# Kernel tuning notes

Hardware: AMD Instinct MI355X
Metric: run time of the kernel (lower is better)

The kernel has to match this reference:

```python
import jax, jax.numpy as jnp
import numpy as np

N_NODES = 50000
N_EDGES = 800000
IN_DIM = 128
OUT_DIM = 64
BN_EPS = 1e-5
LRELU_SLOPE = 0.01


def setup_inputs() -> dict:
    key = jax.random.key(0)
    ks = jax.random.split(key, 8)
    feature = jax.random.normal(ks[0], (N_NODES, IN_DIM), dtype=jnp.float32)
    src = jax.random.randint(ks[1], (N_EDGES,), 0, N_NODES)
    dst = jax.random.randint(ks[2], (N_EDGES,), 0, N_NODES)
    edge_weight = jax.random.uniform(ks[3], (N_EDGES,), dtype=jnp.float32)
    # learned params
    b1 = jnp.zeros((IN_DIM,), jnp.float32)                      # gcn1 bias (weight=False)
    gamma1 = jnp.ones((IN_DIM,), jnp.float32)
    beta1 = jnp.zeros((IN_DIM,), jnp.float32)
    W2 = jax.random.normal(ks[4], (IN_DIM, OUT_DIM), jnp.float32) * (2.0 / IN_DIM) ** 0.5  # kaiming-ish
    b2 = jnp.zeros((OUT_DIM,), jnp.float32)
    gamma2 = jnp.ones((OUT_DIM,), jnp.float32)
    beta2 = jnp.zeros((OUT_DIM,), jnp.float32)
    return dict(feature=feature, edge_weight=edge_weight, b1=b1, gamma1=gamma1,
                beta1=beta1, W2=W2, b2=b2, gamma2=gamma2, beta2=beta2,
                src=src, dst=dst)


def _degrees(src, dst, n):
    ones = jnp.ones(src.shape[0], jnp.float32)
    deg_out = jnp.clip(jax.ops.segment_sum(ones, src, num_segments=n), 1.0)
    deg_in = jnp.clip(jax.ops.segment_sum(ones, dst, num_segments=n), 1.0)
    return deg_out, deg_in


def _graph_conv(x, src, dst, edge_w, W, b, deg_out, deg_in):
    # DGL GraphConv, norm='both': D_in^{-1/2} * A(_w) * D_out^{-1/2} * x (@ W) + b
    h = x * jax.lax.rsqrt(deg_out)[:, None]
    if W is not None:
        h = h @ W  # [N, out]
    m = h[src]                                   # gather  [E, d]
    if edge_w is not None:
        m = m * edge_w[:, None]
    agg = jax.ops.segment_sum(m, dst, num_segments=x.shape[0])  # scatter-add [N, d]
    return agg * jax.lax.rsqrt(deg_in)[:, None] + b


def _batchnorm(x, gamma, beta):
    mean = jnp.mean(x, axis=0)
    var = jnp.var(x, axis=0)  # biased, as torch BN training-mode normalization
    return gamma * (x - mean) * jax.lax.rsqrt(var + BN_EPS) + beta


def reference(feature, edge_weight, b1, gamma1, beta1, W2, b2, gamma2, beta2, src, dst):
    deg_out, deg_in = _degrees(src, dst, feature.shape[0])
    h = _graph_conv(feature, src, dst, edge_weight, None, b1, deg_out, deg_in)
    h = _batchnorm(h, gamma1, beta1)              # dropout = identity (eval)
    h1 = jnp.where(h > 0, h, LRELU_SLOPE * h)     # LeakyReLU
    h2 = _graph_conv(h1, src, dst, None, W2, b2, deg_out, deg_in)
    h = _batchnorm(h2, gamma2, beta2)
    return jax.nn.softmax(h, axis=-1)
```

## Files before the change

### kernel.cpp

```cpp
#include <hip/hip_runtime.h>
#include <cstddef>

typedef unsigned int u32;

#define N_NODES 50000
#define N_EDGES 800000
#define D1 128
#define D2 64
#define BN_EPS 1e-5f
#define LRELU 0.01f
#define ELLW 64
#define C1B 4096
#define C2B 4096

__device__ __forceinline__ u32 f2bf(float x) {
    u32 u = __float_as_uint(x);
    return (u + 0x7fffu + ((u >> 16) & 1u)) >> 16;
}
__device__ __forceinline__ float bflo(u32 p) { return __uint_as_float(p << 16); }
__device__ __forceinline__ float bfhi(u32 p) { return __uint_as_float(p & 0xffff0000u); }

__global__ void k_build(const int* __restrict__ src, const int* __restrict__ dst,
                        const float* __restrict__ ew, const float* __restrict__ feature,
                        int* __restrict__ cnt_in, int* __restrict__ cnt_out,
                        u32* __restrict__ ell, u32* __restrict__ feat_bf) {
    const int e = blockIdx.x * 256 + threadIdx.x;
    if (e < N_EDGES) {
        int d = dst[e];
        int slot = atomicAdd(&cnt_in[d], 1);
        if (slot < ELLW)
            ell[(size_t)d * ELLW + slot] = ((u32)src[e] << 16) | f2bf(ew[e]);
        atomicAdd(&cnt_out[src[e]], 1);
    }
    const int TOTU = N_NODES * (D1 / 2);
    for (int i = e; i < TOTU; i += N_EDGES) {
        float2 v = *(const float2*)&feature[2 * (size_t)i];
        feat_bf[i] = f2bf(v.x) | (f2bf(v.y) << 16);
    }
}

__global__ __launch_bounds__(128) void k_conv1(const u32* __restrict__ feat_bf,
                                               const int* __restrict__ cnt_in,
                                               const int* __restrict__ cnt_out,
                                               const u32* __restrict__ ell,
                                               const float* __restrict__ b1,
                                               float* __restrict__ t1,
                                               float* __restrict__ part1) {
    const int w = threadIdx.x >> 6, lane = threadIdx.x & 63;
    __shared__ int   s_idx[2][ELLW];
    __shared__ float s_sc[2][ELLW];
    __shared__ float red[2][D1];
    const float bb0 = b1[2 * lane], bb1 = b1[2 * lane + 1];
    float s0 = 0.f, q0 = 0.f, s1 = 0.f, q1 = 0.f;
    int cnt = cnt_in[blockIdx.x * 2 + w];
    int deg = min(cnt, ELLW);
    int  pf_i = 0; float pf_c = 0.f;
    if (lane < deg) {
        u32 ent = ell[(size_t)(blockIdx.x * 2 + w) * ELLW + lane];
        pf_i = ent >> 16;
        pf_c = bflo(ent) * rsqrtf((float)max(cnt_out[ent >> 16], 1));
    }
    for (int base = blockIdx.x * 2; base < N_NODES; base += 2 * C1B) {
        const int node = base + w;
        const int cdeg = deg, ccnt = cnt;
        if (lane < cdeg) { s_idx[w][lane] = pf_i; s_sc[w][lane] = pf_c; }
        const int nbase = base + 2 * C1B;
        if (nbase < N_NODES) {
            const int nnode = nbase + w;
            cnt = cnt_in[nnode];
            deg = min(cnt, ELLW);
            if (lane < deg) {
                u32 ent = ell[(size_t)nnode * ELLW + lane];
                pf_i = ent >> 16;
                pf_c = bflo(ent) * rsqrtf((float)max(cnt_out[ent >> 16], 1));
            }
        }
        float a0 = 0.f, a1 = 0.f, a2 = 0.f, a3 = 0.f;
        float a4 = 0.f, a5 = 0.f, a6 = 0.f, a7 = 0.f;
        int j = 0;
        for (; j + 7 < cdeg; j += 8) {
            u32 p0 = feat_bf[(size_t)s_idx[w][j]     * (D1 / 2) + lane];
            u32 p1 = feat_bf[(size_t)s_idx[w][j + 1] * (D1 / 2) + lane];
            u32 p2 = feat_bf[(size_t)s_idx[w][j + 2] * (D1 / 2) + lane];
            u32 p3 = feat_bf[(size_t)s_idx[w][j + 3] * (D1 / 2) + lane];
            u32 p4 = feat_bf[(size_t)s_idx[w][j + 4] * (D1 / 2) + lane];
            u32 p5 = feat_bf[(size_t)s_idx[w][j + 5] * (D1 / 2) + lane];
            u32 p6 = feat_bf[(size_t)s_idx[w][j + 6] * (D1 / 2) + lane];
            u32 p7 = feat_bf[(size_t)s_idx[w][j + 7] * (D1 / 2) + lane];
            float c0 = s_sc[w][j],     c1 = s_sc[w][j + 1];
            float c2 = s_sc[w][j + 2], c3 = s_sc[w][j + 3];
            float c4 = s_sc[w][j + 4], c5 = s_sc[w][j + 5];
            float c6 = s_sc[w][j + 6], c7 = s_sc[w][j + 7];
            a0 = fmaf(bflo(p0), c0, a0); a1 = fmaf(bfhi(p0), c0, a1);
            a2 = fmaf(bflo(p1), c1, a2); a3 = fmaf(bfhi(p1), c1, a3);
            a4 = fmaf(bflo(p2), c2, a4); a5 = fmaf(bfhi(p2), c2, a5);
            a6 = fmaf(bflo(p3), c3, a6); a7 = fmaf(bfhi(p3), c3, a7);
            a0 = fmaf(bflo(p4), c4, a0); a1 = fmaf(bfhi(p4), c4, a1);
            a2 = fmaf(bflo(p5), c5, a2); a3 = fmaf(bfhi(p5), c5, a3);
            a4 = fmaf(bflo(p6), c6, a4); a5 = fmaf(bfhi(p6), c6, a5);
            a6 = fmaf(bflo(p7), c7, a6); a7 = fmaf(bfhi(p7), c7, a7);
        }
        for (; j + 3 < cdeg; j += 4) {
            u32 p0 = feat_bf[(size_t)s_idx[w][j]     * (D1 / 2) + lane];
            u32 p1 = feat_bf[(size_t)s_idx[w][j + 1] * (D1 / 2) + lane];
            u32 p2 = feat_bf[(size_t)s_idx[w][j + 2] * (D1 / 2) + lane];
            u32 p3 = feat_bf[(size_t)s_idx[w][j + 3] * (D1 / 2) + lane];
            float c0 = s_sc[w][j],     c1 = s_sc[w][j + 1];
            float c2 = s_sc[w][j + 2], c3 = s_sc[w][j + 3];
            a0 = fmaf(bflo(p0), c0, a0); a1 = fmaf(bfhi(p0), c0, a1);
            a2 = fmaf(bflo(p1), c1, a2); a3 = fmaf(bfhi(p1), c1, a3);
            a4 = fmaf(bflo(p2), c2, a4); a5 = fmaf(bfhi(p2), c2, a5);
            a6 = fmaf(bflo(p3), c3, a6); a7 = fmaf(bfhi(p3), c3, a7);
        }
        for (; j < cdeg; ++j) {
            u32 p = feat_bf[(size_t)s_idx[w][j] * (D1 / 2) + lane];
            float c = s_sc[w][j];
            a0 = fmaf(bflo(p), c, a0); a1 = fmaf(bfhi(p), c, a1);
        }
        a0 += a2 + a4 + a6;
        a1 += a3 + a5 + a7;
        float r = rsqrtf((float)max(ccnt, 1));
        float v0 = a0 * r + bb0, v1 = a1 * r + bb1;
        float2 v = {v0, v1};
        *(float2*)&t1[(size_t)node * D1 + 2 * lane] = v;
        s0 += v0; q0 += v0 * v0; s1 += v1; q1 += v1 * v1;
    }
    red[w][2 * lane] = s0; red[w][2 * lane + 1] = s1;
    __syncthreads();
    if (w == 0) {
        part1[(size_t)blockIdx.x * 2 * D1 + 2 * lane]     = red[0][2 * lane] + red[1][2 * lane];
        part1[(size_t)blockIdx.x * 2 * D1 + 2 * lane + 1] = red[0][2 * lane + 1] + red[1][2 * lane + 1];
    }
    __syncthreads();
    red[w][2 * lane] = q0; red[w][2 * lane + 1] = q1;
    __syncthreads();
    if (w == 0) {
        part1[(size_t)blockIdx.x * 2 * D1 + D1 + 2 * lane]     = red[0][2 * lane] + red[1][2 * lane];
        part1[(size_t)blockIdx.x * 2 * D1 + D1 + 2 * lane + 1] = red[0][2 * lane + 1] + red[1][2 * lane + 1];
    }
}

template <int D>
__global__ __launch_bounds__(128) void k_bn_final(const float* __restrict__ part, int nblk,
                                                  const float* __restrict__ gamma,
                                                  const float* __restrict__ beta,
                                                  float* __restrict__ coef) {
    const int c = blockIdx.x;
    const int t = threadIdx.x;
    __shared__ float sh[4];
    float s = 0.f, q = 0.f;
    for (int b = t; b < nblk; b += 128) {
        s += part[(size_t)b * 2 * D + c];
        q += part[(size_t)b * 2 * D + D + c];
    }
    for (int o = 32; o >= 1; o >>= 1) {
        s += __shfl_xor(s, o, 64);
        q += __shfl_xor(q, o, 64);
    }
    if ((t & 63) == 0) { sh[(t >> 6) * 2] = s; sh[(t >> 6) * 2 + 1] = q; }
    __syncthreads();
    if (t == 0) {
        s = sh[0] + sh[2];
        q = sh[1] + sh[3];
        const float inv_n = 1.f / (float)N_NODES;
        float mean = s * inv_n;
        float var  = q * inv_n - mean * mean;
        float rstd = rsqrtf(var + BN_EPS);
        float a = gamma[c] * rstd;
        coef[c]     = a;
        coef[D + c] = beta[c] - mean * a;
    }
}

__global__ __launch_bounds__(256) void k_mm(const float* __restrict__ t1,
                                            const float* __restrict__ coef1,
                                            const int* __restrict__ cnt_out,
                                            const float* __restrict__ W2,
                                            u32* __restrict__ g_bf) {
    __shared__ float sW[D1 * D2];
    __shared__ float sX[32][132];
    const int tid = threadIdx.x;
    const int r0 = blockIdx.x * 32;
    for (int i = tid; i < D1 * D2 / 4; i += 256)
        ((float4*)sW)[i] = ((const float4*)W2)[i];
    for (int i = tid; i < 32 * (D1 / 4); i += 256) {
        int r = i >> 5, k4 = i & 31;
        int row = r0 + r;
        float4 v = {0.f, 0.f, 0.f, 0.f};
        if (row < N_NODES) {
            v = *(const float4*)&t1[(size_t)row * D1 + 4 * k4];
            float ro = rsqrtf((float)max(cnt_out[row], 1));
            int k = 4 * k4;
            float x;
            x = coef1[k]     * v.x + coef1[D1 + k];     v.x = ((x > 0.f) ? x : LRELU * x) * ro;
            x = coef1[k + 1] * v.y + coef1[D1 + k + 1]; v.y = ((x > 0.f) ? x : LRELU * x) * ro;
            x = coef1[k + 2] * v.z + coef1[D1 + k + 2]; v.z = ((x > 0.f) ? x : LRELU * x) * ro;
            x = coef1[k + 3] * v.w + coef1[D1 + k + 3]; v.w = ((x > 0.f) ? x : LRELU * x) * ro;
        }
        *(float4*)&sX[r][4 * k4] = v;
    }
    __syncthreads();
    const int c  = tid & 63;
    const int rg = tid >> 6;
    float acc[8] = {0.f, 0.f, 0.f, 0.f, 0.f, 0.f, 0.f, 0.f};
    for (int k = 0; k < D1; k += 4) {
        float w0 = sW[k * D2 + c];
        float w1 = sW[(k + 1) * D2 + c];
        float w2 = sW[(k + 2) * D2 + c];
        float w3 = sW[(k + 3) * D2 + c];
#pragma unroll
        for (int j = 0; j < 8; ++j) {
            float4 x4 = *(const float4*)&sX[rg + 4 * j][k];
            acc[j] = fmaf(x4.x, w0, acc[j]);
            acc[j] = fmaf(x4.y, w1, acc[j]);
            acc[j] = fmaf(x4.z, w2, acc[j]);
            acc[j] = fmaf(x4.w, w3, acc[j]);
        }
    }
#pragma unroll
    for (int j = 0; j < 8; ++j) {
        int row = r0 + rg + 4 * j;
        float partner = __shfl_xor(acc[j], 1, 64);
        if (row < N_NODES && (c & 1) == 0)
            g_bf[(size_t)row * (D2 / 2) + (c >> 1)] = f2bf(acc[j]) | (f2bf(partner) << 16);
    }
}

__global__ __launch_bounds__(128) void k_conv2(const u32* __restrict__ g_bf,
                                               const int* __restrict__ cnt_in,
                                               const u32* __restrict__ ell,
                                               const float* __restrict__ b2,
                                               float* __restrict__ out,
                                               float* __restrict__ part2) {
    const int w = threadIdx.x >> 6, lane = threadIdx.x & 63;
    const int m = lane & 31, half = lane >> 5;
    __shared__ int   s_idx[2][ELLW];
    __shared__ float red[2][D2];
    const float bb0 = b2[2 * m], bb1 = b2[2 * m + 1];
    float s0 = 0.f, q0 = 0.f, s1 = 0.f, q1 = 0.f;
    int cnt = cnt_in[blockIdx.x * 2 + w];
    int deg = min(cnt, ELLW);
    int pf_i = 0;
    if (lane < deg) pf_i = ell[(size_t)(blockIdx.x * 2 + w) * ELLW + lane] >> 16;
    for (int base = blockIdx.x * 2; base < N_NODES; base += 2 * C2B) {
        const int node = base + w;
        const int cdeg = deg, ccnt = cnt;
        if (lane < cdeg) s_idx[w][lane] = pf_i;
        const int nbase = base + 2 * C2B;
        if (nbase < N_NODES) {
            const int nnode = nbase + w;
            cnt = cnt_in[nnode];
            deg = min(cnt, ELLW);
            if (lane < deg) pf_i = ell[(size_t)nnode * ELLW + lane] >> 16;
        }
        float a0 = 0.f, a1 = 0.f, a2 = 0.f, a3 = 0.f;
        float a4 = 0.f, a5 = 0.f, a6 = 0.f, a7 = 0.f;
        int j = half;
        for (; j + 14 < cdeg; j += 16) {
            u32 p0 = g_bf[(size_t)s_idx[w][j]      * (D2 / 2) + m];
            u32 p1 = g_bf[(size_t)s_idx[w][j + 2]  * (D2 / 2) + m];
            u32 p2 = g_bf[(size_t)s_idx[w][j + 4]  * (D2 / 2) + m];
            u32 p3 = g_bf[(size_t)s_idx[w][j + 6]  * (D2 / 2) + m];
            u32 p4 = g_bf[(size_t)s_idx[w][j + 8]  * (D2 / 2) + m];
            u32 p5 = g_bf[(size_t)s_idx[w][j + 10] * (D2 / 2) + m];
            u32 p6 = g_bf[(size_t)s_idx[w][j + 12] * (D2 / 2) + m];
            u32 p7 = g_bf[(size_t)s_idx[w][j + 14] * (D2 / 2) + m];
            a0 += bflo(p0); a1 += bfhi(p0);
            a2 += bflo(p1); a3 += bfhi(p1);
            a4 += bflo(p2); a5 += bfhi(p2);
            a6 += bflo(p3); a7 += bfhi(p3);
            a0 += bflo(p4); a1 += bfhi(p4);
            a2 += bflo(p5); a3 += bfhi(p5);
            a4 += bflo(p6); a5 += bfhi(p6);
            a6 += bflo(p7); a7 += bfhi(p7);
        }
        for (; j + 6 < cdeg; j += 8) {
            u32 p0 = g_bf[(size_t)s_idx[w][j]     * (D2 / 2) + m];
            u32 p1 = g_bf[(size_t)s_idx[w][j + 2] * (D2 / 2) + m];
            u32 p2 = g_bf[(size_t)s_idx[w][j + 4] * (D2 / 2) + m];
            u32 p3 = g_bf[(size_t)s_idx[w][j + 6] * (D2 / 2) + m];
            a0 += bflo(p0); a1 += bfhi(p0);
            a2 += bflo(p1); a3 += bfhi(p1);
            a4 += bflo(p2); a5 += bfhi(p2);
            a6 += bflo(p3); a7 += bfhi(p3);
        }
        for (; j < cdeg; j += 2) {
            u32 p = g_bf[(size_t)s_idx[w][j] * (D2 / 2) + m];
            a0 += bflo(p); a1 += bfhi(p);
        }
        a0 += a2 + a4 + a6;
        a1 += a3 + a5 + a7;
        a0 += __shfl_xor(a0, 32, 64);
        a1 += __shfl_xor(a1, 32, 64);
        float r = rsqrtf((float)max(ccnt, 1));
        float v0 = a0 * r + bb0, v1 = a1 * r + bb1;
        if (half == 0) {
            float2 v = {v0, v1};
            *(float2*)&out[(size_t)node * D2 + 2 * m] = v;
            s0 += v0; q0 += v0 * v0; s1 += v1; q1 += v1 * v1;
        }
    }
    if (half == 0) { red[w][2 * m] = s0; red[w][2 * m + 1] = s1; }
    __syncthreads();
    if (w == 0 && half == 0) {
        part2[(size_t)blockIdx.x * 2 * D2 + 2 * m]     = red[0][2 * m] + red[1][2 * m];
        part2[(size_t)blockIdx.x * 2 * D2 + 2 * m + 1] = red[0][2 * m + 1] + red[1][2 * m + 1];
    }
    __syncthreads();
    if (half == 0) { red[w][2 * m] = q0; red[w][2 * m + 1] = q1; }
    __syncthreads();
    if (w == 0 && half == 0) {
        part2[(size_t)blockIdx.x * 2 * D2 + D2 + 2 * m]     = red[0][2 * m] + red[1][2 * m];
        part2[(size_t)blockIdx.x * 2 * D2 + D2 + 2 * m + 1] = red[0][2 * m + 1] + red[1][2 * m + 1];
    }
}

__global__ __launch_bounds__(256) void k_softmax(float* __restrict__ out,
                                                 const float* __restrict__ coef2) {
    const int tid = threadIdx.x;
    const int lane = tid & 63;
    const int row = blockIdx.x * 4 + (tid >> 6);
    if (row >= N_NODES) return;
    float v = out[(size_t)row * D2 + lane] * coef2[lane] + coef2[D2 + lane];
    float m = v;
    for (int o = 32; o >= 1; o >>= 1) m = fmaxf(m, __shfl_xor(m, o, 64));
    float e = expf(v - m);
    float s = e;
    for (int o = 32; o >= 1; o >>= 1) s += __shfl_xor(s, o, 64);
    out[(size_t)row * D2 + lane] = e / s;
}

extern "C" void kernel_launch(void* const* d_in, const int* in_sizes, int n_in,
                              void* d_out, int out_size, void* d_ws, size_t ws_size,
                              hipStream_t stream) {
    const float* feature = (const float*)d_in[0];
    const float* edge_w  = (const float*)d_in[1];
    const float* b1      = (const float*)d_in[2];
    const float* gamma1  = (const float*)d_in[3];
    const float* beta1   = (const float*)d_in[4];
    const float* W2      = (const float*)d_in[5];
    const float* b2      = (const float*)d_in[6];
    const float* gamma2  = (const float*)d_in[7];
    const float* beta2   = (const float*)d_in[8];
    const int*   src     = (const int*)d_in[9];
    const int*   dst     = (const int*)d_in[10];

    float* out = (float*)d_out;

    int*   cnt_in  = (int*)d_ws;
    int*   cnt_out = cnt_in + 50000;
    float* coef1   = (float*)(cnt_out + 50000);
    float* coef2   = coef1 + 256;
    float* part1   = coef2 + 128;
    u32*   ell     = (u32*)(part1 + 1048576);
    float* t1      = (float*)(ell + (size_t)N_NODES * ELLW);
    u32*   feat_bf = (u32*)(t1 + (size_t)N_NODES * D1);
    u32*   g_bf    = feat_bf;
    float* part2   = part1;

    hipMemsetAsync(cnt_in, 0, 2 * 50000 * sizeof(int), stream);

    const int EB = (N_EDGES + 255) / 256;
    k_build<<<EB, 256, 0, stream>>>(src, dst, edge_w, feature,
                                    cnt_in, cnt_out, ell, feat_bf);

    k_conv1<<<C1B, 128, 0, stream>>>(feat_bf, cnt_in, cnt_out, ell, b1, t1, part1);
    k_bn_final<D1><<<D1, 128, 0, stream>>>(part1, C1B, gamma1, beta1, coef1);

    k_mm<<<(N_NODES + 31) / 32, 256, 0, stream>>>(t1, coef1, cnt_out, W2, g_bf);

    k_conv2<<<C2B, 128, 0, stream>>>(g_bf, cnt_in, ell, b2, out, part2);
    k_bn_final<D2><<<D2, 128, 0, stream>>>(part2, C2B, gamma2, beta2, coef2);

    k_softmax<<<(N_NODES + 3) / 4, 256, 0, stream>>>(out, coef2);
}
```

Baseline: 210.8 us.

## Fuse conv1, BN, matmul, conv2 and softmax into one cooperative kernel

Replaces six separate launches (conv1, two BN finalizers, matmul, conv2, softmax) with one persistent cooperative kernel of 1024 blocks that separates the phases with grid-wide syncs. The goal is to remove per-launch overhead and launch gaps, and to shrink the partial-sum buffers, since BN now reduces over 1024 blocks instead of 4096. In exchange the grid is smaller, so per-block occupancy and latency hiding are lower. Grid syncs also add their own cost, the matmul tile shrinks to 8 rows, and the large static LDS allocation may limit how many blocks fit per CU.

```diff
diff --git a/kernel.cpp b/kernel.cpp
--- a/kernel.cpp
+++ b/kernel.cpp
@@ -1,6 +1,8 @@
 #include <hip/hip_runtime.h>
+#include <hip/hip_cooperative_groups.h>
 #include <cstddef>
 
+namespace cg = cooperative_groups;
 typedef unsigned int u32;
 
 #define N_NODES 50000
@@ -10,8 +12,7 @@
 #define BN_EPS 1e-5f
 #define LRELU 0.01f
 #define ELLW 64
-#define C1B 4096
-#define C2B 4096
+#define GRID 1024
 
 __device__ __forceinline__ u32 f2bf(float x) {
     u32 u = __float_as_uint(x);
@@ -39,129 +40,20 @@
     }
 }
 
-__global__ __launch_bounds__(128) void k_conv1(const u32* __restrict__ feat_bf,
-                                               const int* __restrict__ cnt_in,
-                                               const int* __restrict__ cnt_out,
-                                               const u32* __restrict__ ell,
-                                               const float* __restrict__ b1,
-                                               float* __restrict__ t1,
-                                               float* __restrict__ part1) {
-    const int w = threadIdx.x >> 6, lane = threadIdx.x & 63;
-    __shared__ int   s_idx[2][ELLW];
-    __shared__ float s_sc[2][ELLW];
-    __shared__ float red[2][D1];
-    const float bb0 = b1[2 * lane], bb1 = b1[2 * lane + 1];
-    float s0 = 0.f, q0 = 0.f, s1 = 0.f, q1 = 0.f;
-    int cnt = cnt_in[blockIdx.x * 2 + w];
-    int deg = min(cnt, ELLW);
-    int  pf_i = 0; float pf_c = 0.f;
-    if (lane < deg) {
-        u32 ent = ell[(size_t)(blockIdx.x * 2 + w) * ELLW + lane];
-        pf_i = ent >> 16;
-        pf_c = bflo(ent) * rsqrtf((float)max(cnt_out[ent >> 16], 1));
-    }
-    for (int base = blockIdx.x * 2; base < N_NODES; base += 2 * C1B) {
-        const int node = base + w;
-        const int cdeg = deg, ccnt = cnt;
-        if (lane < cdeg) { s_idx[w][lane] = pf_i; s_sc[w][lane] = pf_c; }
-        const int nbase = base + 2 * C1B;
-        if (nbase < N_NODES) {
-            const int nnode = nbase + w;
-            cnt = cnt_in[nnode];
-            deg = min(cnt, ELLW);
-            if (lane < deg) {
-                u32 ent = ell[(size_t)nnode * ELLW + lane];
-                pf_i = ent >> 16;
-                pf_c = bflo(ent) * rsqrtf((float)max(cnt_out[ent >> 16], 1));
-            }
-        }
-        float a0 = 0.f, a1 = 0.f, a2 = 0.f, a3 = 0.f;
-        float a4 = 0.f, a5 = 0.f, a6 = 0.f, a7 = 0.f;
-        int j = 0;
-        for (; j + 7 < cdeg; j += 8) {
-            u32 p0 = feat_bf[(size_t)s_idx[w][j]     * (D1 / 2) + lane];
-            u32 p1 = feat_bf[(size_t)s_idx[w][j + 1] * (D1 / 2) + lane];
-            u32 p2 = feat_bf[(size_t)s_idx[w][j + 2] * (D1 / 2) + lane];
-            u32 p3 = feat_bf[(size_t)s_idx[w][j + 3] * (D1 / 2) + lane];
-            u32 p4 = feat_bf[(size_t)s_idx[w][j + 4] * (D1 / 2) + lane];
-            u32 p5 = feat_bf[(size_t)s_idx[w][j + 5] * (D1 / 2) + lane];
-            u32 p6 = feat_bf[(size_t)s_idx[w][j + 6] * (D1 / 2) + lane];
-            u32 p7 = feat_bf[(size_t)s_idx[w][j + 7] * (D1 / 2) + lane];
-            float c0 = s_sc[w][j],     c1 = s_sc[w][j + 1];
-            float c2 = s_sc[w][j + 2], c3 = s_sc[w][j + 3];
-            float c4 = s_sc[w][j + 4], c5 = s_sc[w][j + 5];
-            float c6 = s_sc[w][j + 6], c7 = s_sc[w][j + 7];
-            a0 = fmaf(bflo(p0), c0, a0); a1 = fmaf(bfhi(p0), c0, a1);
-            a2 = fmaf(bflo(p1), c1, a2); a3 = fmaf(bfhi(p1), c1, a3);
-            a4 = fmaf(bflo(p2), c2, a4); a5 = fmaf(bfhi(p2), c2, a5);
-            a6 = fmaf(bflo(p3), c3, a6); a7 = fmaf(bfhi(p3), c3, a7);
-            a0 = fmaf(bflo(p4), c4, a0); a1 = fmaf(bfhi(p4), c4, a1);
-            a2 = fmaf(bflo(p5), c5, a2); a3 = fmaf(bfhi(p5), c5, a3);
-            a4 = fmaf(bflo(p6), c6, a4); a5 = fmaf(bfhi(p6), c6, a5);
-            a6 = fmaf(bflo(p7), c7, a6); a7 = fmaf(bfhi(p7), c7, a7);
-        }
-        for (; j + 3 < cdeg; j += 4) {
-            u32 p0 = feat_bf[(size_t)s_idx[w][j]     * (D1 / 2) + lane];
-            u32 p1 = feat_bf[(size_t)s_idx[w][j + 1] * (D1 / 2) + lane];
-            u32 p2 = feat_bf[(size_t)s_idx[w][j + 2] * (D1 / 2) + lane];
-            u32 p3 = feat_bf[(size_t)s_idx[w][j + 3] * (D1 / 2) + lane];
-            float c0 = s_sc[w][j],     c1 = s_sc[w][j + 1];
-            float c2 = s_sc[w][j + 2], c3 = s_sc[w][j + 3];
-            a0 = fmaf(bflo(p0), c0, a0); a1 = fmaf(bfhi(p0), c0, a1);
-            a2 = fmaf(bflo(p1), c1, a2); a3 = fmaf(bfhi(p1), c1, a3);
-            a4 = fmaf(bflo(p2), c2, a4); a5 = fmaf(bfhi(p2), c2, a5);
-            a6 = fmaf(bflo(p3), c3, a6); a7 = fmaf(bfhi(p3), c3, a7);
-        }
-        for (; j < cdeg; ++j) {
-            u32 p = feat_bf[(size_t)s_idx[w][j] * (D1 / 2) + lane];
-            float c = s_sc[w][j];
-            a0 = fmaf(bflo(p), c, a0); a1 = fmaf(bfhi(p), c, a1);
-        }
-        a0 += a2 + a4 + a6;
-        a1 += a3 + a5 + a7;
-        float r = rsqrtf((float)max(ccnt, 1));
-        float v0 = a0 * r + bb0, v1 = a1 * r + bb1;
-        float2 v = {v0, v1};
-        *(float2*)&t1[(size_t)node * D1 + 2 * lane] = v;
-        s0 += v0; q0 += v0 * v0; s1 += v1; q1 += v1 * v1;
-    }
-    red[w][2 * lane] = s0; red[w][2 * lane + 1] = s1;
-    __syncthreads();
-    if (w == 0) {
-        part1[(size_t)blockIdx.x * 2 * D1 + 2 * lane]     = red[0][2 * lane] + red[1][2 * lane];
-        part1[(size_t)blockIdx.x * 2 * D1 + 2 * lane + 1] = red[0][2 * lane + 1] + red[1][2 * lane + 1];
-    }
-    __syncthreads();
-    red[w][2 * lane] = q0; red[w][2 * lane + 1] = q1;
-    __syncthreads();
-    if (w == 0) {
-        part1[(size_t)blockIdx.x * 2 * D1 + D1 + 2 * lane]     = red[0][2 * lane] + red[1][2 * lane];
-        part1[(size_t)blockIdx.x * 2 * D1 + D1 + 2 * lane + 1] = red[0][2 * lane + 1] + red[1][2 * lane + 1];
-    }
-}
-
-template <int D>
-__global__ __launch_bounds__(128) void k_bn_final(const float* __restrict__ part, int nblk,
-                                                  const float* __restrict__ gamma,
-                                                  const float* __restrict__ beta,
-                                                  float* __restrict__ coef) {
-    const int c = blockIdx.x;
-    const int t = threadIdx.x;
-    __shared__ float sh[4];
+__device__ __forceinline__ void bnf_dev(const float* part, int nblk,
+                                        const float* gamma, const float* beta,
+                                        float* coef, int D, float* sh) {
+    const int c = blockIdx.x, t = threadIdx.x;
     float s = 0.f, q = 0.f;
     for (int b = t; b < nblk; b += 128) {
         s += part[(size_t)b * 2 * D + c];
         q += part[(size_t)b * 2 * D + D + c];
     }
-    for (int o = 32; o >= 1; o >>= 1) {
-        s += __shfl_xor(s, o, 64);
-        q += __shfl_xor(q, o, 64);
-    }
+    for (int o = 32; o >= 1; o >>= 1) { s += __shfl_xor(s, o, 64); q += __shfl_xor(q, o, 64); }
     if ((t & 63) == 0) { sh[(t >> 6) * 2] = s; sh[(t >> 6) * 2 + 1] = q; }
     __syncthreads();
     if (t == 0) {
-        s = sh[0] + sh[2];
-        q = sh[1] + sh[3];
+        s = sh[0] + sh[2]; q = sh[1] + sh[3];
         const float inv_n = 1.f / (float)N_NODES;
         float mean = s * inv_n;
         float var  = q * inv_n - mean * mean;
@@ -172,162 +64,287 @@
     }
 }
 
-__global__ __launch_bounds__(256) void k_mm(const float* __restrict__ t1,
-                                            const float* __restrict__ coef1,
-                                            const int* __restrict__ cnt_out,
-                                            const float* __restrict__ W2,
-                                            u32* __restrict__ g_bf) {
-    __shared__ float sW[D1 * D2];
-    __shared__ float sX[32][132];
+#define LDSB (32768 + 8 * 132 * 4)
+
+__global__ __launch_bounds__(128) void k_mega(const u32* __restrict__ feat_bf,
+                                              const int* __restrict__ cnt_in,
+                                              const int* __restrict__ cnt_out,
+                                              const u32* __restrict__ ell,
+                                              const float* __restrict__ b1,
+                                              float* __restrict__ t1,
+                                              float* __restrict__ part1,
+                                              const float* __restrict__ gamma1,
+                                              const float* __restrict__ beta1,
+                                              float* __restrict__ coef1,
+                                              const float* __restrict__ W2,
+                                              u32* __restrict__ g_bf,
+                                              const float* __restrict__ b2,
+                                              float* __restrict__ out,
+                                              float* __restrict__ part2,
+                                              const float* __restrict__ gamma2,
+                                              const float* __restrict__ beta2,
+                                              float* __restrict__ coef2) {
+    cg::grid_group grid = cg::this_grid();
+    __shared__ __align__(16) char lds[LDSB];
     const int tid = threadIdx.x;
-    const int r0 = blockIdx.x * 32;
-    for (int i = tid; i < D1 * D2 / 4; i += 256)
-        ((float4*)sW)[i] = ((const float4*)W2)[i];
-    for (int i = tid; i < 32 * (D1 / 4); i += 256) {
-        int r = i >> 5, k4 = i & 31;
-        int row = r0 + r;
-        float4 v = {0.f, 0.f, 0.f, 0.f};
-        if (row < N_NODES) {
-            v = *(const float4*)&t1[(size_t)row * D1 + 4 * k4];
-            float ro = rsqrtf((float)max(cnt_out[row], 1));
-            int k = 4 * k4;
-            float x;
-            x = coef1[k]     * v.x + coef1[D1 + k];     v.x = ((x > 0.f) ? x : LRELU * x) * ro;
-            x = coef1[k + 1] * v.y + coef1[D1 + k + 1]; v.y = ((x > 0.f) ? x : LRELU * x) * ro;
-            x = coef1[k + 2] * v.z + coef1[D1 + k + 2]; v.z = ((x > 0.f) ? x : LRELU * x) * ro;
-            x = coef1[k + 3] * v.w + coef1[D1 + k + 3]; v.w = ((x > 0.f) ? x : LRELU * x) * ro;
-        }
-        *(float4*)&sX[r][4 * k4] = v;
-    }
-    __syncthreads();
-    const int c  = tid & 63;
-    const int rg = tid >> 6;
-    float acc[8] = {0.f, 0.f, 0.f, 0.f, 0.f, 0.f, 0.f, 0.f};
-    for (int k = 0; k < D1; k += 4) {
-        float w0 = sW[k * D2 + c];
-        float w1 = sW[(k + 1) * D2 + c];
-        float w2 = sW[(k + 2) * D2 + c];
-        float w3 = sW[(k + 3) * D2 + c];
-#pragma unroll
-        for (int j = 0; j < 8; ++j) {
-            float4 x4 = *(const float4*)&sX[rg + 4 * j][k];
-            acc[j] = fmaf(x4.x, w0, acc[j]);
-            acc[j] = fmaf(x4.y, w1, acc[j]);
-            acc[j] = fmaf(x4.z, w2, acc[j]);
-            acc[j] = fmaf(x4.w, w3, acc[j]);
-        }
-    }
-#pragma unroll
-    for (int j = 0; j < 8; ++j) {
-        int row = r0 + rg + 4 * j;
-        float partner = __shfl_xor(acc[j], 1, 64);
-        if (row < N_NODES && (c & 1) == 0)
-            g_bf[(size_t)row * (D2 / 2) + (c >> 1)] = f2bf(acc[j]) | (f2bf(partner) << 16);
-    }
-}
-
-__global__ __launch_bounds__(128) void k_conv2(const u32* __restrict__ g_bf,
-                                               const int* __restrict__ cnt_in,
-                                               const u32* __restrict__ ell,
-                                               const float* __restrict__ b2,
-                                               float* __restrict__ out,
-                                               float* __restrict__ part2) {
-    const int w = threadIdx.x >> 6, lane = threadIdx.x & 63;
-    const int m = lane & 31, half = lane >> 5;
-    __shared__ int   s_idx[2][ELLW];
-    __shared__ float red[2][D2];
-    const float bb0 = b2[2 * m], bb1 = b2[2 * m + 1];
-    float s0 = 0.f, q0 = 0.f, s1 = 0.f, q1 = 0.f;
-    int cnt = cnt_in[blockIdx.x * 2 + w];
-    int deg = min(cnt, ELLW);
-    int pf_i = 0;
-    if (lane < deg) pf_i = ell[(size_t)(blockIdx.x * 2 + w) * ELLW + lane] >> 16;
-    for (int base = blockIdx.x * 2; base < N_NODES; base += 2 * C2B) {
-        const int node = base + w;
-        const int cdeg = deg, ccnt = cnt;
-        if (lane < cdeg) s_idx[w][lane] = pf_i;
-        const int nbase = base + 2 * C2B;
-        if (nbase < N_NODES) {
-            const int nnode = nbase + w;
-            cnt = cnt_in[nnode];
-            deg = min(cnt, ELLW);
-            if (lane < deg) pf_i = ell[(size_t)nnode * ELLW + lane] >> 16;
-        }
-        float a0 = 0.f, a1 = 0.f, a2 = 0.f, a3 = 0.f;
-        float a4 = 0.f, a5 = 0.f, a6 = 0.f, a7 = 0.f;
-        int j = half;
-        for (; j + 14 < cdeg; j += 16) {
-            u32 p0 = g_bf[(size_t)s_idx[w][j]      * (D2 / 2) + m];
-            u32 p1 = g_bf[(size_t)s_idx[w][j + 2]  * (D2 / 2) + m];
-            u32 p2 = g_bf[(size_t)s_idx[w][j + 4]  * (D2 / 2) + m];
-            u32 p3 = g_bf[(size_t)s_idx[w][j + 6]  * (D2 / 2) + m];
-            u32 p4 = g_bf[(size_t)s_idx[w][j + 8]  * (D2 / 2) + m];
-            u32 p5 = g_bf[(size_t)s_idx[w][j + 10] * (D2 / 2) + m];
-            u32 p6 = g_bf[(size_t)s_idx[w][j + 12] * (D2 / 2) + m];
-            u32 p7 = g_bf[(size_t)s_idx[w][j + 14] * (D2 / 2) + m];
-            a0 += bflo(p0); a1 += bfhi(p0);
-            a2 += bflo(p1); a3 += bfhi(p1);
-            a4 += bflo(p2); a5 += bfhi(p2);
-            a6 += bflo(p3); a7 += bfhi(p3);
-            a0 += bflo(p4); a1 += bfhi(p4);
-            a2 += bflo(p5); a3 += bfhi(p5);
-            a4 += bflo(p6); a5 += bfhi(p6);
-            a6 += bflo(p7); a7 += bfhi(p7);
-        }
-        for (; j + 6 < cdeg; j += 8) {
-            u32 p0 = g_bf[(size_t)s_idx[w][j]     * (D2 / 2) + m];
-            u32 p1 = g_bf[(size_t)s_idx[w][j + 2] * (D2 / 2) + m];
-            u32 p2 = g_bf[(size_t)s_idx[w][j + 4] * (D2 / 2) + m];
-            u32 p3 = g_bf[(size_t)s_idx[w][j + 6] * (D2 / 2) + m];
-            a0 += bflo(p0); a1 += bfhi(p0);
-            a2 += bflo(p1); a3 += bfhi(p1);
-            a4 += bflo(p2); a5 += bfhi(p2);
-            a6 += bflo(p3); a7 += bfhi(p3);
-        }
-        for (; j < cdeg; j += 2) {
-            u32 p = g_bf[(size_t)s_idx[w][j] * (D2 / 2) + m];
-            a0 += bflo(p); a1 += bfhi(p);
-        }
-        a0 += a2 + a4 + a6;
-        a1 += a3 + a5 + a7;
-        a0 += __shfl_xor(a0, 32, 64);
-        a1 += __shfl_xor(a1, 32, 64);
-        float r = rsqrtf((float)max(ccnt, 1));
-        float v0 = a0 * r + bb0, v1 = a1 * r + bb1;
-        if (half == 0) {
+    const int w = tid >> 6, lane = tid & 63;
+
+    {
+        int*   s_idx = (int*)lds;
+        float* s_sc  = (float*)(lds + 512);
+        float* red   = (float*)(lds + 1024);
+        const float bb0 = b1[2 * lane], bb1 = b1[2 * lane + 1];
+        float s0 = 0.f, q0 = 0.f, s1 = 0.f, q1 = 0.f;
+        int cnt = cnt_in[blockIdx.x * 2 + w];
+        int deg = min(cnt, ELLW);
+        int pf_i = 0; float pf_c = 0.f;
+        if (lane < deg) {
+            u32 ent = ell[(size_t)(blockIdx.x * 2 + w) * ELLW + lane];
+            pf_i = ent >> 16;
+            pf_c = bflo(ent) * rsqrtf((float)max(cnt_out[ent >> 16], 1));
+        }
+        for (int base = blockIdx.x * 2; base < N_NODES; base += 2 * GRID) {
+            const int node = base + w;
+            const int cdeg = deg, ccnt = cnt;
+            if (lane < cdeg) { s_idx[w * ELLW + lane] = pf_i; s_sc[w * ELLW + lane] = pf_c; }
+            const int nbase = base + 2 * GRID;
+            if (nbase < N_NODES) {
+                const int nnode = nbase + w;
+                cnt = cnt_in[nnode];
+                deg = min(cnt, ELLW);
+                if (lane < deg) {
+                    u32 ent = ell[(size_t)nnode * ELLW + lane];
+                    pf_i = ent >> 16;
+                    pf_c = bflo(ent) * rsqrtf((float)max(cnt_out[ent >> 16], 1));
+                }
+            }
+            float a0 = 0.f, a1 = 0.f, a2 = 0.f, a3 = 0.f;
+            float a4 = 0.f, a5 = 0.f, a6 = 0.f, a7 = 0.f;
+            int j = 0;
+            for (; j + 7 < cdeg; j += 8) {
+                u32 p0 = feat_bf[(size_t)s_idx[w * ELLW + j]     * (D1 / 2) + lane];
+                u32 p1 = feat_bf[(size_t)s_idx[w * ELLW + j + 1] * (D1 / 2) + lane];
+                u32 p2 = feat_bf[(size_t)s_idx[w * ELLW + j + 2] * (D1 / 2) + lane];
+                u32 p3 = feat_bf[(size_t)s_idx[w * ELLW + j + 3] * (D1 / 2) + lane];
+                u32 p4 = feat_bf[(size_t)s_idx[w * ELLW + j + 4] * (D1 / 2) + lane];
+                u32 p5 = feat_bf[(size_t)s_idx[w * ELLW + j + 5] * (D1 / 2) + lane];
+                u32 p6 = feat_bf[(size_t)s_idx[w * ELLW + j + 6] * (D1 / 2) + lane];
+                u32 p7 = feat_bf[(size_t)s_idx[w * ELLW + j + 7] * (D1 / 2) + lane];
+                float c0 = s_sc[w * ELLW + j],     c1 = s_sc[w * ELLW + j + 1];
+                float c2 = s_sc[w * ELLW + j + 2], c3 = s_sc[w * ELLW + j + 3];
+                float c4 = s_sc[w * ELLW + j + 4], c5 = s_sc[w * ELLW + j + 5];
+                float c6 = s_sc[w * ELLW + j + 6], c7 = s_sc[w * ELLW + j + 7];
+                a0 = fmaf(bflo(p0), c0, a0); a1 = fmaf(bfhi(p0), c0, a1);
+                a2 = fmaf(bflo(p1), c1, a2); a3 = fmaf(bfhi(p1), c1, a3);
+                a4 = fmaf(bflo(p2), c2, a4); a5 = fmaf(bfhi(p2), c2, a5);
+                a6 = fmaf(bflo(p3), c3, a6); a7 = fmaf(bfhi(p3), c3, a7);
+                a0 = fmaf(bflo(p4), c4, a0); a1 = fmaf(bfhi(p4), c4, a1);
+                a2 = fmaf(bflo(p5), c5, a2); a3 = fmaf(bfhi(p5), c5, a3);
+                a4 = fmaf(bflo(p6), c6, a4); a5 = fmaf(bfhi(p6), c6, a5);
+                a6 = fmaf(bflo(p7), c7, a6); a7 = fmaf(bfhi(p7), c7, a7);
+            }
+            for (; j + 3 < cdeg; j += 4) {
+                u32 p0 = feat_bf[(size_t)s_idx[w * ELLW + j]     * (D1 / 2) + lane];
+                u32 p1 = feat_bf[(size_t)s_idx[w * ELLW + j + 1] * (D1 / 2) + lane];
+                u32 p2 = feat_bf[(size_t)s_idx[w * ELLW + j + 2] * (D1 / 2) + lane];
+                u32 p3 = feat_bf[(size_t)s_idx[w * ELLW + j + 3] * (D1 / 2) + lane];
+                float c0 = s_sc[w * ELLW + j],     c1 = s_sc[w * ELLW + j + 1];
+                float c2 = s_sc[w * ELLW + j + 2], c3 = s_sc[w * ELLW + j + 3];
+                a0 = fmaf(bflo(p0), c0, a0); a1 = fmaf(bfhi(p0), c0, a1);
+                a2 = fmaf(bflo(p1), c1, a2); a3 = fmaf(bfhi(p1), c1, a3);
+                a4 = fmaf(bflo(p2), c2, a4); a5 = fmaf(bfhi(p2), c2, a5);
+                a6 = fmaf(bflo(p3), c3, a6); a7 = fmaf(bfhi(p3), c3, a7);
+            }
+            for (; j < cdeg; ++j) {
+                u32 p = feat_bf[(size_t)s_idx[w * ELLW + j] * (D1 / 2) + lane];
+                float c = s_sc[w * ELLW + j];
+                a0 = fmaf(bflo(p), c, a0); a1 = fmaf(bfhi(p), c, a1);
+            }
+            a0 += a2 + a4 + a6;
+            a1 += a3 + a5 + a7;
+            float r = rsqrtf((float)max(ccnt, 1));
+            float v0 = a0 * r + bb0, v1 = a1 * r + bb1;
             float2 v = {v0, v1};
-            *(float2*)&out[(size_t)node * D2 + 2 * m] = v;
+            *(float2*)&t1[(size_t)node * D1 + 2 * lane] = v;
             s0 += v0; q0 += v0 * v0; s1 += v1; q1 += v1 * v1;
         }
-    }
-    if (half == 0) { red[w][2 * m] = s0; red[w][2 * m + 1] = s1; }
-    __syncthreads();
-    if (w == 0 && half == 0) {
-        part2[(size_t)blockIdx.x * 2 * D2 + 2 * m]     = red[0][2 * m] + red[1][2 * m];
-        part2[(size_t)blockIdx.x * 2 * D2 + 2 * m + 1] = red[0][2 * m + 1] + red[1][2 * m + 1];
-    }
-    __syncthreads();
-    if (half == 0) { red[w][2 * m] = q0; red[w][2 * m + 1] = q1; }
-    __syncthreads();
-    if (w == 0 && half == 0) {
-        part2[(size_t)blockIdx.x * 2 * D2 + D2 + 2 * m]     = red[0][2 * m] + red[1][2 * m];
-        part2[(size_t)blockIdx.x * 2 * D2 + D2 + 2 * m + 1] = red[0][2 * m + 1] + red[1][2 * m + 1];
-    }
-}
-
-__global__ __launch_bounds__(256) void k_softmax(float* __restrict__ out,
-                                                 const float* __restrict__ coef2) {
-    const int tid = threadIdx.x;
-    const int lane = tid & 63;
-    const int row = blockIdx.x * 4 + (tid >> 6);
-    if (row >= N_NODES) return;
-    float v = out[(size_t)row * D2 + lane] * coef2[lane] + coef2[D2 + lane];
-    float m = v;
-    for (int o = 32; o >= 1; o >>= 1) m = fmaxf(m, __shfl_xor(m, o, 64));
-    float e = expf(v - m);
-    float s = e;
-    for (int o = 32; o >= 1; o >>= 1) s += __shfl_xor(s, o, 64);
-    out[(size_t)row * D2 + lane] = e / s;
+        red[w * D1 + 2 * lane] = s0; red[w * D1 + 2 * lane + 1] = s1;
+        __syncthreads();
+        if (w == 0) {
+            part1[(size_t)blockIdx.x * 2 * D1 + 2 * lane]     = red[2 * lane] + red[D1 + 2 * lane];
+            part1[(size_t)blockIdx.x * 2 * D1 + 2 * lane + 1] = red[2 * lane + 1] + red[D1 + 2 * lane + 1];
+        }
+        __syncthreads();
+        red[w * D1 + 2 * lane] = q0; red[w * D1 + 2 * lane + 1] = q1;
+        __syncthreads();
+        if (w == 0) {
+            part1[(size_t)blockIdx.x * 2 * D1 + D1 + 2 * lane]     = red[2 * lane] + red[D1 + 2 * lane];
+            part1[(size_t)blockIdx.x * 2 * D1 + D1 + 2 * lane + 1] = red[2 * lane + 1] + red[D1 + 2 * lane + 1];
+        }
+    }
+    grid.sync();
+
+    if (blockIdx.x < D1) bnf_dev(part1, GRID, gamma1, beta1, coef1, D1, (float*)lds);
+    grid.sync();
+
+    {
+        float* sW = (float*)lds;
+        float (*sx)[132] = (float(*)[132])(lds + 32768);
+        for (int i = tid; i < D1 * D2 / 4; i += 128)
+            ((float4*)sW)[i] = ((const float4*)W2)[i];
+        __syncthreads();
+        const int c = lane;
+        for (int t = blockIdx.x; t < N_NODES / 8; t += GRID) {
+            const int r0 = t * 8;
+            for (int i = tid; i < 8 * (D1 / 4); i += 128) {
+                int r = i >> 5, k4 = i & 31;
+                int row = r0 + r;
+                float4 v = *(const float4*)&t1[(size_t)row * D1 + 4 * k4];
+                float ro = rsqrtf((float)max(cnt_out[row], 1));
+                int k = 4 * k4;
+                float x;
+                x = coef1[k]     * v.x + coef1[D1 + k];     v.x = ((x > 0.f) ? x : LRELU * x) * ro;
+                x = coef1[k + 1] * v.y + coef1[D1 + k + 1]; v.y = ((x > 0.f) ? x : LRELU * x) * ro;
+                x = coef1[k + 2] * v.z + coef1[D1 + k + 2]; v.z = ((x > 0.f) ? x : LRELU * x) * ro;
+                x = coef1[k + 3] * v.w + coef1[D1 + k + 3]; v.w = ((x > 0.f) ? x : LRELU * x) * ro;
+                *(float4*)&sx[r][4 * k4] = v;
+            }
+            __syncthreads();
+            float acc0 = 0.f, acc1 = 0.f, acc2 = 0.f, acc3 = 0.f;
+            const int rb = w * 4;
+            for (int k = 0; k < D1; k += 4) {
+                float w0 = sW[k * D2 + c];
+                float w1 = sW[(k + 1) * D2 + c];
+                float w2 = sW[(k + 2) * D2 + c];
+                float w3 = sW[(k + 3) * D2 + c];
+                float4 x0 = *(const float4*)&sx[rb][k];
+                float4 x1 = *(const float4*)&sx[rb + 1][k];
+                float4 x2 = *(const float4*)&sx[rb + 2][k];
+                float4 x3 = *(const float4*)&sx[rb + 3][k];
+                acc0 = fmaf(x0.x, w0, acc0); acc0 = fmaf(x0.y, w1, acc0);
+                acc0 = fmaf(x0.z, w2, acc0); acc0 = fmaf(x0.w, w3, acc0);
+                acc1 = fmaf(x1.x, w0, acc1); acc1 = fmaf(x1.y, w1, acc1);
+                acc1 = fmaf(x1.z, w2, acc1); acc1 = fmaf(x1.w, w3, acc1);
+                acc2 = fmaf(x2.x, w0, acc2); acc2 = fmaf(x2.y, w1, acc2);
+                acc2 = fmaf(x2.z, w2, acc2); acc2 = fmaf(x2.w, w3, acc2);
+                acc3 = fmaf(x3.x, w0, acc3); acc3 = fmaf(x3.y, w1, acc3);
+                acc3 = fmaf(x3.z, w2, acc3); acc3 = fmaf(x3.w, w3, acc3);
+            }
+            float p0 = __shfl_xor(acc0, 1, 64);
+            float p1 = __shfl_xor(acc1, 1, 64);
+            float p2 = __shfl_xor(acc2, 1, 64);
+            float p3 = __shfl_xor(acc3, 1, 64);
+            if ((c & 1) == 0) {
+                g_bf[(size_t)(r0 + rb)     * (D2 / 2) + (c >> 1)] = f2bf(acc0) | (f2bf(p0) << 16);
+                g_bf[(size_t)(r0 + rb + 1) * (D2 / 2) + (c >> 1)] = f2bf(acc1) | (f2bf(p1) << 16);
+                g_bf[(size_t)(r0 + rb + 2) * (D2 / 2) + (c >> 1)] = f2bf(acc2) | (f2bf(p2) << 16);
+                g_bf[(size_t)(r0 + rb + 3) * (D2 / 2) + (c >> 1)] = f2bf(acc3) | (f2bf(p3) << 16);
+            }
+            __syncthreads();
+        }
+    }
+    grid.sync();
+
+    {
+        int*   s_idx = (int*)lds;
+        float* red   = (float*)(lds + 512);
+        const int m = lane & 31, half = lane >> 5;
+        const float bb0 = b2[2 * m], bb1 = b2[2 * m + 1];
+        float s0 = 0.f, q0 = 0.f, s1 = 0.f, q1 = 0.f;
+        int cnt = cnt_in[blockIdx.x * 2 + w];
+        int deg = min(cnt, ELLW);
+        int pf_i = 0;
+        if (lane < deg) pf_i = ell[(size_t)(blockIdx.x * 2 + w) * ELLW + lane] >> 16;
+        for (int base = blockIdx.x * 2; base < N_NODES; base += 2 * GRID) {
+            const int node = base + w;
+            const int cdeg = deg, ccnt = cnt;
+            if (lane < cdeg) s_idx[w * ELLW + lane] = pf_i;
+            const int nbase = base + 2 * GRID;
+            if (nbase < N_NODES) {
+                const int nnode = nbase + w;
+                cnt = cnt_in[nnode];
+                deg = min(cnt, ELLW);
+                if (lane < deg) pf_i = ell[(size_t)nnode * ELLW + lane] >> 16;
+            }
+            float a0 = 0.f, a1 = 0.f, a2 = 0.f, a3 = 0.f;
+            float a4 = 0.f, a5 = 0.f, a6 = 0.f, a7 = 0.f;
+            int j = half;
+            for (; j + 14 < cdeg; j += 16) {
+                u32 p0 = g_bf[(size_t)s_idx[w * ELLW + j]      * (D2 / 2) + m];
+                u32 p1 = g_bf[(size_t)s_idx[w * ELLW + j + 2]  * (D2 / 2) + m];
+                u32 p2 = g_bf[(size_t)s_idx[w * ELLW + j + 4]  * (D2 / 2) + m];
+                u32 p3 = g_bf[(size_t)s_idx[w * ELLW + j + 6]  * (D2 / 2) + m];
+                u32 p4 = g_bf[(size_t)s_idx[w * ELLW + j + 8]  * (D2 / 2) + m];
+                u32 p5 = g_bf[(size_t)s_idx[w * ELLW + j + 10] * (D2 / 2) + m];
+                u32 p6 = g_bf[(size_t)s_idx[w * ELLW + j + 12] * (D2 / 2) + m];
+                u32 p7 = g_bf[(size_t)s_idx[w * ELLW + j + 14] * (D2 / 2) + m];
+                a0 += bflo(p0); a1 += bfhi(p0);
+                a2 += bflo(p1); a3 += bfhi(p1);
+                a4 += bflo(p2); a5 += bfhi(p2);
+                a6 += bflo(p3); a7 += bfhi(p3);
+                a0 += bflo(p4); a1 += bfhi(p4);
+                a2 += bflo(p5); a3 += bfhi(p5);
+                a4 += bflo(p6); a5 += bfhi(p6);
+                a6 += bflo(p7); a7 += bfhi(p7);
+            }
+            for (; j + 6 < cdeg; j += 8) {
+                u32 p0 = g_bf[(size_t)s_idx[w * ELLW + j]     * (D2 / 2) + m];
+                u32 p1 = g_bf[(size_t)s_idx[w * ELLW + j + 2] * (D2 / 2) + m];
+                u32 p2 = g_bf[(size_t)s_idx[w * ELLW + j + 4] * (D2 / 2) + m];
+                u32 p3 = g_bf[(size_t)s_idx[w * ELLW + j + 6] * (D2 / 2) + m];
+                a0 += bflo(p0); a1 += bfhi(p0);
+                a2 += bflo(p1); a3 += bfhi(p1);
+                a4 += bflo(p2); a5 += bfhi(p2);
+                a6 += bflo(p3); a7 += bfhi(p3);
+            }
+            for (; j < cdeg; j += 2) {
+                u32 p = g_bf[(size_t)s_idx[w * ELLW + j] * (D2 / 2) + m];
+                a0 += bflo(p); a1 += bfhi(p);
+            }
+            a0 += a2 + a4 + a6;
+            a1 += a3 + a5 + a7;
+            a0 += __shfl_xor(a0, 32, 64);
+            a1 += __shfl_xor(a1, 32, 64);
+            float r = rsqrtf((float)max(ccnt, 1));
+            float v0 = a0 * r + bb0, v1 = a1 * r + bb1;
+            if (half == 0) {
+                float2 v = {v0, v1};
+                *(float2*)&out[(size_t)node * D2 + 2 * m] = v;
+                s0 += v0; q0 += v0 * v0; s1 += v1; q1 += v1 * v1;
+            }
+        }
+        if (half == 0) { red[w * D2 + 2 * m] = s0; red[w * D2 + 2 * m + 1] = s1; }
+        __syncthreads();
+        if (w == 0 && half == 0) {
+            part2[(size_t)blockIdx.x * 2 * D2 + 2 * m]     = red[2 * m] + red[D2 + 2 * m];
+            part2[(size_t)blockIdx.x * 2 * D2 + 2 * m + 1] = red[2 * m + 1] + red[D2 + 2 * m + 1];
+        }
+        __syncthreads();
+        if (half == 0) { red[w * D2 + 2 * m] = q0; red[w * D2 + 2 * m + 1] = q1; }
+        __syncthreads();
+        if (w == 0 && half == 0) {
+            part2[(size_t)blockIdx.x * 2 * D2 + D2 + 2 * m]     = red[2 * m] + red[D2 + 2 * m];
+            part2[(size_t)blockIdx.x * 2 * D2 + D2 + 2 * m + 1] = red[2 * m + 1] + red[D2 + 2 * m + 1];
+        }
+    }
+    grid.sync();
+
+    if (blockIdx.x < D2) bnf_dev(part2, GRID, gamma2, beta2, coef2, D2, (float*)lds);
+    grid.sync();
+
+    {
+        const float ca = coef2[lane & 63];
+        const float cb = coef2[D2 + (lane & 63)];
+        for (int row = blockIdx.x * 2 + w; row < N_NODES; row += 2 * GRID) {
+            float v = out[(size_t)row * D2 + lane] * ca + cb;
+            float mx = v;
+            for (int o = 32; o >= 1; o >>= 1) mx = fmaxf(mx, __shfl_xor(mx, o, 64));
+            float e = expf(v - mx);
+            float s = e;
+            for (int o = 32; o >= 1; o >>= 1) s += __shfl_xor(s, o, 64);
+            out[(size_t)row * D2 + lane] = e / s;
+        }
+    }
 }
 
 extern "C" void kernel_launch(void* const* d_in, const int* in_sizes, int n_in,
@@ -352,7 +369,7 @@
     float* coef1   = (float*)(cnt_out + 50000);
     float* coef2   = coef1 + 256;
     float* part1   = coef2 + 128;
-    u32*   ell     = (u32*)(part1 + 1048576);
+    u32*   ell     = (u32*)(part1 + (size_t)GRID * 2 * D1);
     float* t1      = (float*)(ell + (size_t)N_NODES * ELLW);
     u32*   feat_bf = (u32*)(t1 + (size_t)N_NODES * D1);
     u32*   g_bf    = feat_bf;
@@ -364,13 +381,10 @@
     k_build<<<EB, 256, 0, stream>>>(src, dst, edge_w, feature,
                                     cnt_in, cnt_out, ell, feat_bf);
 
-    k_conv1<<<C1B, 128, 0, stream>>>(feat_bf, cnt_in, cnt_out, ell, b1, t1, part1);
-    k_bn_final<D1><<<D1, 128, 0, stream>>>(part1, C1B, gamma1, beta1, coef1);
-
-    k_mm<<<(N_NODES + 31) / 32, 256, 0, stream>>>(t1, coef1, cnt_out, W2, g_bf);
-
-    k_conv2<<<C2B, 128, 0, stream>>>(g_bf, cnt_in, ell, b2, out, part2);
-    k_bn_final<D2><<<D2, 128, 0, stream>>>(part2, C2B, gamma2, beta2, coef2);
-
-    k_softmax<<<(N_NODES + 3) / 4, 256, 0, stream>>>(out, coef2);
-}
+    void* args[] = { (void*)&feat_bf, (void*)&cnt_in, (void*)&cnt_out, (void*)&ell,
+                     (void*)&b1, (void*)&t1, (void*)&part1,
+                     (void*)&gamma1, (void*)&beta1, (void*)&coef1,
+                     (void*)&W2, (void*)&g_bf, (void*)&b2, (void*)&out, (void*)&part2,
+                     (void*)&gamma2, (void*)&beta2, (void*)&coef2 };
+    hipLaunchCooperativeKernel((const void*)k_mega, dim3(GRID), dim3(128), args, 0, stream);
+}
```

New measurement: 808.2 us. +283.5%, slower.
